# Performance work log

Hardware: AMD Instinct MI355X
Metric: run time of the kernel (lower is better)

## Reference

```python
import jax, jax.numpy as jnp
import numpy as np

S, B, D, H, E, K = 1024, 4, 1024, 16, 3, 2
DFF = 4 * D
DH = D // H


def _layernorm(x, w, b, eps=1e-5):
    mu = jnp.mean(x, axis=-1, keepdims=True)
    var = jnp.var(x, axis=-1, keepdims=True)
    return (x - mu) * jax.lax.rsqrt(var + eps) * w + b


def _quick_gelu(x):
    return x * jax.nn.sigmoid(1.702 * x)


def setup_inputs() -> dict:
    key = jax.random.key(0)
    ks = jax.random.split(key, 8)
    w = lambda k, shape: jax.random.normal(k, shape, dtype=jnp.float32) * 0.02
    return {
        "x": jax.random.normal(ks[0], (S, B, D), dtype=jnp.float32),
        "ln1_w": jnp.ones((D,), jnp.float32), "ln1_b": jnp.zeros((D,), jnp.float32),
        "ln2_w": jnp.ones((D,), jnp.float32), "ln2_b": jnp.zeros((D,), jnp.float32),
        "in_proj_w": w(ks[1], (3 * D, D)), "in_proj_b": jnp.zeros((3 * D,), jnp.float32),
        "out_proj_w": w(ks[2], (D, D)), "out_proj_b": jnp.zeros((D,), jnp.float32),
        "gate_w": w(ks[3], (E, D)),
        "fc_w": w(ks[4], (E, DFF, D)), "fc_b": jnp.zeros((E, DFF), jnp.float32),
        "proj_w": w(ks[5], (E, D, DFF)), "proj_b": jnp.zeros((E, D), jnp.float32),
    }


def _forward(x, ln1_w, ln1_b, ln2_w, ln2_b, in_proj_w, in_proj_b,
             out_proj_w, out_proj_b, gate_w, fc_w, fc_b, proj_w, proj_b):
    s, b, d = x.shape
    # --- causal self-attention (torch nn.MultiheadAttention, seq-first) ---
    h = _layernorm(x, ln1_w, ln1_b)
    qkv = h @ in_proj_w.T + in_proj_b                      # [S,B,3D]
    q, k, v = jnp.split(qkv, 3, axis=-1)
    to_bhsd = lambda t: t.reshape(s, b, H, DH).transpose(1, 2, 0, 3)  # [B,H,S,Dh]
    q, k, v = to_bhsd(q) * (DH ** -0.5), to_bhsd(k), to_bhsd(v)
    mask = jnp.where(jnp.arange(s)[:, None] >= jnp.arange(s)[None, :], 0.0, -jnp.inf)
    scores = jnp.einsum("bhqd,bhkd->bhqk", q, k) + mask    # [B,H,S,S]
    attn = jax.nn.softmax(scores, axis=-1)
    o = jnp.einsum("bhqk,bhkd->bhqd", attn, v)
    o = o.transpose(2, 0, 1, 3).reshape(s, b, d)
    x = x + (o @ out_proj_w.T + out_proj_b)

    # --- MoE routing ---
    hs = _layernorm(x, ln2_w, ln2_b)
    hs_flat = hs.reshape(-1, d)                            # [T,D], T = S*B
    router_logits = hs_flat @ gate_w.T                     # [T,E]
    rw = jax.nn.softmax(router_logits.astype(jnp.float32), axis=-1)
    top_vals, top_idx = jax.lax.top_k(rw, K)               # [T,K]
    top_vals = top_vals / jnp.sum(top_vals, axis=-1, keepdims=True)

    # dense grouped expert FFN (E=3 small, compute-all + masked combine)
    h1 = _quick_gelu(jnp.einsum("td,efd->etf", hs_flat, fc_w) + fc_b[:, None, :])
    expert_out = jnp.einsum("etf,edf->etd", h1, proj_w) + proj_b[:, None, :]  # [E,T,D]
    comb = jnp.sum(jax.nn.one_hot(top_idx, E, dtype=top_vals.dtype) * top_vals[..., None], axis=1)  # [T,E]
    final_hidden_states = jnp.einsum("te,etd->td", comb, expert_out).reshape(s, b, d)
    del final_hidden_states  # NOTE: source computes this but never uses it in the output

    gate_score = jnp.max(top_vals, axis=-1).reshape(s, b, 1)
    out = x * gate_score
    return out, router_logits


def reference(x, ln1_w, ln1_b, ln2_w, ln2_b, in_proj_w, in_proj_b,
              out_proj_w, out_proj_b, gate_w, fc_w, fc_b, proj_w, proj_b):
    return _forward(x, ln1_w, ln1_b, ln2_w, ln2_b, in_proj_w, in_proj_b,
                    out_proj_w, out_proj_b, gate_w, fc_w, fc_b, proj_w, proj_b)
```

## Files before the change

### kernel.cpp

```cpp
#include <hip/hip_runtime.h>
#include <hip/hip_bf16.h>

#define S_DIM 1024
#define B_DIM 4
#define D_DIM 1024
#define H_DIM 16
#define DH    64
#define T_DIM (S_DIM * B_DIM)
#define QKV_N (3 * D_DIM)

using bf16 = __hip_bfloat16;
typedef __attribute__((ext_vector_type(4))) float fx4;
typedef __attribute__((ext_vector_type(8))) short bx8;

__device__ __forceinline__ unsigned short f2bf(float f) {
  union { float f; unsigned int u; } cv; cv.f = f;
  unsigned int u = cv.u;
  unsigned int r = (u + 0x7FFFu + ((u >> 16) & 1u)) >> 16;
  return (unsigned short)r;
}

__device__ __forceinline__ void g2l16(const void* g, void* l) {
  __builtin_amdgcn_global_load_lds(
      (const __attribute__((address_space(1))) unsigned int*)g,
      (__attribute__((address_space(3))) unsigned int*)l, 16, 0, 0);
}

__global__ __launch_bounds__(256) void cast_f32_bf16(
    const float* __restrict__ src, bf16* __restrict__ dst, int n4) {
  const int i = blockIdx.x * 256 + threadIdx.x;
  if (i >= n4) return;
  const fx4 v = ((const fx4*)src)[i];
  ushort4 u;
  u.x = f2bf(v[0]); u.y = f2bf(v[1]); u.z = f2bf(v[2]); u.w = f2bf(v[3]);
  ((ushort4*)dst)[i] = u;
}

__global__ __launch_bounds__(256) void ln_bf16_kernel(
    const float* __restrict__ x, const float* __restrict__ w,
    const float* __restrict__ bb, bf16* __restrict__ out) {
  const int t = blockIdx.x, tid = threadIdx.x;
  const fx4 v = ((const fx4*)(x + (size_t)t * D_DIM))[tid];
  float s  = v[0] + v[1] + v[2] + v[3];
  float ss = v[0]*v[0] + v[1]*v[1] + v[2]*v[2] + v[3]*v[3];
#pragma unroll
  for (int off = 32; off >= 1; off >>= 1) {
    s  += __shfl_xor(s, off);
    ss += __shfl_xor(ss, off);
  }
  __shared__ float red[8];
  const int wid = tid >> 6, lane = tid & 63;
  if (lane == 0) { red[wid] = s; red[4 + wid] = ss; }
  __syncthreads();
  s  = red[0] + red[1] + red[2] + red[3];
  ss = red[4] + red[5] + red[6] + red[7];
  const float mu = s * (1.f / D_DIM);
  const float rstd = rsqrtf(ss * (1.f / D_DIM) - mu * mu + 1e-5f);
  const fx4 wv = ((const fx4*)w)[tid];
  const fx4 bv = ((const fx4*)bb)[tid];
  ushort4 u;
  u.x = f2bf((v[0] - mu) * rstd * wv[0] + bv[0]);
  u.y = f2bf((v[1] - mu) * rstd * wv[1] + bv[1]);
  u.z = f2bf((v[2] - mu) * rstd * wv[2] + bv[2]);
  u.w = f2bf((v[3] - mu) * rstd * wv[3] + bv[3]);
  ((ushort4*)(out + (size_t)t * D_DIM))[tid] = u;
}

template <int EPI>
__global__ __launch_bounds__(256, 2) void gemm_bt(
    const bf16* __restrict__ A, const bf16* __restrict__ B,
    const float* __restrict__ bias, const float* __restrict__ resid,
    float* __restrict__ C, ushort* __restrict__ qkvb, int N, int K) {
  __shared__ bf16 sA[128 * 32];
  __shared__ bf16 sB[128 * 32];
  const int tid  = threadIdx.x;
  const int brow = blockIdx.y * 128;
  const int bcol = blockIdx.x * 128;
  const int wid  = tid >> 6;
  const int lane = tid & 63;
  const int wr   = wid >> 1;
  const int wc   = wid & 1;
  const int fr   = lane & 15;
  const int fk   = lane >> 4;

  fx4 acc[4][4];
#pragma unroll
  for (int i = 0; i < 4; ++i)
#pragma unroll
    for (int j = 0; j < 4; ++j) acc[i][j] = 0.f;

  const int arow = tid >> 2;
  const int acol = (tid & 3) * 8;

  for (int kt = 0; kt < K; kt += 32) {
    __syncthreads();
#pragma unroll
    for (int is = 0; is < 2; ++is) {
      const int row = is * 64 + arow;
      const int off = row * 64 + acol * 2;
      g2l16(A + (size_t)(brow + row) * K + kt + acol, (char*)sA + off);
      g2l16(B + (size_t)(bcol + row) * K + kt + acol, (char*)sB + off);
    }
    __syncthreads();

    bx8 af[4], bfr[4];
#pragma unroll
    for (int mm = 0; mm < 4; ++mm)
      af[mm] = *(const bx8*)(sA + (wr * 64 + mm * 16 + fr) * 32 + fk * 8);
#pragma unroll
    for (int nn = 0; nn < 4; ++nn)
      bfr[nn] = *(const bx8*)(sB + (wc * 64 + nn * 16 + fr) * 32 + fk * 8);
#pragma unroll
    for (int mm = 0; mm < 4; ++mm)
#pragma unroll
      for (int nn = 0; nn < 4; ++nn)
        acc[mm][nn] = __builtin_amdgcn_mfma_f32_16x16x32_bf16(
            af[mm], bfr[nn], acc[mm][nn], 0, 0, 0);
  }

  const int row0 = brow + wr * 64 + fk * 4;
  const int col0 = bcol + wc * 64 + fr;
#pragma unroll
  for (int mm = 0; mm < 4; ++mm) {
#pragma unroll
    for (int nn = 0; nn < 4; ++nn) {
      const int col = col0 + nn * 16;
      const float bv = bias[col];
      if (EPI == 1) {
#pragma unroll
        for (int rr = 0; rr < 4; ++rr) {
          const int row = row0 + mm * 16 + rr;
          C[(size_t)row * N + col] = acc[mm][nn][rr] + bv + resid[(size_t)row * N + col];
        }
      } else {
        const int which = col >> 10;
        const int rem   = col & 1023;
        const int hh    = rem >> 6;
        const int dh    = rem & 63;
        const float scale = (which == 0) ? 0.125f : 1.0f;
#pragma unroll
        for (int rr = 0; rr < 4; ++rr) {
          const int row = row0 + mm * 16 + rr;
          const int ss2 = row >> 2, bb2 = row & 3;
          const float v = (acc[mm][nn][rr] + bv) * scale;
          qkvb[(size_t)which * 4194304 +
               ((size_t)(bb2 * 16 + hh)) * 65536 + (size_t)ss2 * 64 + dh] = f2bf(v);
        }
      }
    }
  }
}

__global__ __launch_bounds__(256, 4) void attn_mfma(
    const ushort* __restrict__ qb, const ushort* __restrict__ kb,
    const ushort* __restrict__ vb, ushort* __restrict__ ob) {
  __shared__ __align__(16) char sK[8192];
  __shared__ __align__(16) char sVT[8192];
  __shared__ __align__(16) char sP[8192];
  const int tid  = threadIdx.x;
  const int wid  = tid >> 6;
  const int lane = tid & 63;
  const int g  = blockIdx.x;
  const int u  = g >> 1;
  const int pr = u & 7;
  const int qt = (g & 1) ? (15 - pr) : pr;
  const int bh = u >> 3;
  const int b  = bh >> 4, h = bh & 15;
  const int q0 = qt * 64;
  const int fr = lane & 15;
  const int fk = lane >> 4;
  const size_t bhoff = (size_t)bh * 65536;

  const int qrow = q0 + wid * 16 + fr;
  const bx8 qf0 = *(const bx8*)(qb + bhoff + (size_t)qrow * 64 + fk * 8);
  const bx8 qf1 = *(const bx8*)(qb + bhoff + (size_t)qrow * 64 + 32 + fk * 8);

  fx4 o4[4];
  float m[4], l[4];
#pragma unroll
  for (int dt = 0; dt < 4; ++dt) o4[dt] = 0.f;
#pragma unroll
  for (int rr = 0; rr < 4; ++rr) { m[rr] = -INFINITY; l[rr] = 0.f; }

  char* const sPw = sP + wid * 2048;

  for (int kbk = 0; kbk <= qt; ++kbk) {
    const int k0 = kbk * 64;
    __syncthreads();
#pragma unroll
    for (int is = 0; is < 2; ++is) {
      const int L    = is * 4096 + tid * 16;
      const int row  = L >> 7;
      const int colb = (L & 127) ^ ((row & 7) << 4);
      g2l16(kb + bhoff + (size_t)(k0 + row) * 64 + (colb >> 1), sK + L);
    }
    {
      const ushort* vp = vb + bhoff + (size_t)(k0 + lane) * 64 + wid * 16;
      const bx8 va  = *(const bx8*)vp;
      const bx8 vb2 = *(const bx8*)(vp + 8);
#pragma unroll
      for (int i = 0; i < 8; ++i) {
        const int dh0 = wid * 16 + i;
        *(ushort*)(sVT + ((dh0 * 128 + lane * 2) ^ ((i & 7) << 4))) = (ushort)va[i];
        const int dh1 = dh0 + 8;
        *(ushort*)(sVT + ((dh1 * 128 + lane * 2) ^ ((i & 7) << 4))) = (ushort)vb2[i];
      }
    }
    __syncthreads();

    fx4 s4[4];
#pragma unroll
    for (int kt = 0; kt < 4; ++kt) {
      const int krow = kt * 16 + fr;
      const int sw   = (krow & 7) << 4;
      const bx8 b0 = *(const bx8*)(sK + krow * 128 + ((fk * 16) ^ sw));
      const bx8 b1 = *(const bx8*)(sK + krow * 128 + ((64 + fk * 16) ^ sw));
      fx4 z = {0.f, 0.f, 0.f, 0.f};
      z = __builtin_amdgcn_mfma_f32_16x16x32_bf16(qf0, b0, z, 0, 0, 0);
      s4[kt] = __builtin_amdgcn_mfma_f32_16x16x32_bf16(qf1, b1, z, 0, 0, 0);
    }

    if (kbk == qt) {
#pragma unroll
      for (int kt = 0; kt < 4; ++kt) {
        const int key = k0 + kt * 16 + fr;
#pragma unroll
        for (int rr = 0; rr < 4; ++rr) {
          const int qq = q0 + wid * 16 + fk * 4 + rr;
          if (key > qq) s4[kt][rr] = -INFINITY;
        }
      }
    }

    float pm[4];
#pragma unroll
    for (int rr = 0; rr < 4; ++rr)
      pm[rr] = fmaxf(fmaxf(s4[0][rr], s4[1][rr]), fmaxf(s4[2][rr], s4[3][rr]));
#pragma unroll
    for (int off = 1; off <= 8; off <<= 1)
#pragma unroll
      for (int rr = 0; rr < 4; ++rr)
        pm[rr] = fmaxf(pm[rr], __shfl_xor(pm[rr], off));

#pragma unroll
    for (int rr = 0; rr < 4; ++rr) {
      const float mn = fmaxf(m[rr], pm[rr]);
      const float f  = __expf(m[rr] - mn);
      m[rr] = mn;
      l[rr] *= f;
#pragma unroll
      for (int dt = 0; dt < 4; ++dt) o4[dt][rr] *= f;
    }

#pragma unroll
    for (int kt = 0; kt < 4; ++kt) {
#pragma unroll
      for (int rr = 0; rr < 4; ++rr) {
        const float pv = __expf(s4[kt][rr] - m[rr]);
        l[rr] += pv;
        const int qr = fk * 4 + rr;
        *(ushort*)(sPw + ((qr * 128 + (kt * 16 + fr) * 2) ^ ((qr & 7) << 4))) = f2bf(pv);
      }
    }

#pragma unroll
    for (int c = 0; c < 2; ++c) {
      const bx8 pa = *(const bx8*)(sPw + fr * 128 + ((c * 64 + fk * 16) ^ ((fr & 7) << 4)));
#pragma unroll
      for (int dt = 0; dt < 4; ++dt) {
        const int vrow = dt * 16 + fr;
        const bx8 vf = *(const bx8*)(sVT + vrow * 128 + ((c * 64 + fk * 16) ^ ((vrow & 7) << 4)));
        o4[dt] = __builtin_amdgcn_mfma_f32_16x16x32_bf16(pa, vf, o4[dt], 0, 0, 0);
      }
    }
  }

#pragma unroll
  for (int off = 1; off <= 8; off <<= 1)
#pragma unroll
    for (int rr = 0; rr < 4; ++rr) l[rr] += __shfl_xor(l[rr], off);
#pragma unroll
  for (int rr = 0; rr < 4; ++rr) l[rr] = 1.f / l[rr];

#pragma unroll
  for (int dt = 0; dt < 4; ++dt) {
#pragma unroll
    for (int rr = 0; rr < 4; ++rr) {
      const int qq = q0 + wid * 16 + fk * 4 + rr;
      ob[((size_t)qq * 4 + b) * 1024 + h * 64 + dt * 16 + fr] =
          f2bf(o4[dt][rr] * l[rr]);
    }
  }
}

__global__ __launch_bounds__(256) void final_kernel(
    const float* __restrict__ xn, const float* __restrict__ w,
    const float* __restrict__ bb, const float* __restrict__ gw,
    float* __restrict__ out, float* __restrict__ rlog) {
  const int t = blockIdx.x, tid = threadIdx.x;
  const fx4 v = ((const fx4*)(xn + (size_t)t * D_DIM))[tid];
  float s  = v[0] + v[1] + v[2] + v[3];
  float ss = v[0]*v[0] + v[1]*v[1] + v[2]*v[2] + v[3]*v[3];
#pragma unroll
  for (int off = 32; off >= 1; off >>= 1) {
    s  += __shfl_xor(s, off);
    ss += __shfl_xor(ss, off);
  }
  __shared__ float red[8];
  __shared__ float red2[12];
  const int wid = tid >> 6, lane = tid & 63;
  if (lane == 0) { red[wid] = s; red[4 + wid] = ss; }
  __syncthreads();
  s  = red[0] + red[1] + red[2] + red[3];
  ss = red[4] + red[5] + red[6] + red[7];
  const float mu = s * (1.f / D_DIM);
  const float rstd = rsqrtf(ss * (1.f / D_DIM) - mu * mu + 1e-5f);
  const fx4 wv = ((const fx4*)w)[tid];
  const fx4 bv = ((const fx4*)bb)[tid];
  fx4 hv;
#pragma unroll
  for (int cc = 0; cc < 4; ++cc) hv[cc] = (v[cc] - mu) * rstd * wv[cc] + bv[cc];

  const fx4 w0 = ((const fx4*)(gw           ))[tid];
  const fx4 w1 = ((const fx4*)(gw +     D_DIM))[tid];
  const fx4 w2 = ((const fx4*)(gw + 2 * D_DIM))[tid];
  float g0 = hv[0]*w0[0] + hv[1]*w0[1] + hv[2]*w0[2] + hv[3]*w0[3];
  float g1 = hv[0]*w1[0] + hv[1]*w1[1] + hv[2]*w1[2] + hv[3]*w1[3];
  float g2 = hv[0]*w2[0] + hv[1]*w2[1] + hv[2]*w2[2] + hv[3]*w2[3];
#pragma unroll
  for (int off = 32; off >= 1; off >>= 1) {
    g0 += __shfl_xor(g0, off);
    g1 += __shfl_xor(g1, off);
    g2 += __shfl_xor(g2, off);
  }
  if (lane == 0) { red2[wid] = g0; red2[4 + wid] = g1; red2[8 + wid] = g2; }
  __syncthreads();
  g0 = red2[0] + red2[1] + red2[2]  + red2[3];
  g1 = red2[4] + red2[5] + red2[6]  + red2[7];
  g2 = red2[8] + red2[9] + red2[10] + red2[11];

  const float lmax = fmaxf(g0, fmaxf(g1, g2));
  const float lmin = fminf(g0, fminf(g1, g2));
  const float lmid = (g0 + g1 + g2) - lmax - lmin;
  const float gate = 1.f / (1.f + __expf(lmid - lmax));

  ((fx4*)(out + (size_t)t * D_DIM))[tid] = v * gate;
  if (tid == 0) {
    rlog[(size_t)t * 3 + 0] = g0;
    rlog[(size_t)t * 3 + 1] = g1;
    rlog[(size_t)t * 3 + 2] = g2;
  }
}

extern "C" void kernel_launch(void* const* d_in, const int* in_sizes, int n_in,
                              void* d_out, int out_size, void* d_ws, size_t ws_size,
                              hipStream_t stream) {
  (void)in_sizes; (void)n_in; (void)out_size; (void)ws_size;
  const float* x    = (const float*)d_in[0];
  const float* ln1w = (const float*)d_in[1];
  const float* ln1b = (const float*)d_in[2];
  const float* ln2w = (const float*)d_in[3];
  const float* ln2b = (const float*)d_in[4];
  const float* win  = (const float*)d_in[5];
  const float* bin  = (const float*)d_in[6];
  const float* wout = (const float*)d_in[7];
  const float* bout = (const float*)d_in[8];
  const float* gw   = (const float*)d_in[9];

  char* ws = (char*)d_ws;
  bf16*   w_in_b  = (bf16*)(ws);
  bf16*   w_out_b = (bf16*)(ws + 6291456);
  bf16*   h_b     = (bf16*)(ws + 8388608);
  ushort* o_b     = (ushort*)h_b;
  ushort* qkvb    = (ushort*)(ws + 16777216);
  ushort* q_b     = qkvb;
  ushort* k_b     = qkvb + 4194304;
  ushort* v_b     = qkvb + 8388608;
  float*  xnew    = (float*)(ws + 41943040);

  float* out  = (float*)d_out;
  float* rlog = out + (size_t)T_DIM * D_DIM;

  cast_f32_bf16<<<(3145728 / 4) / 256, 256, 0, stream>>>(win,  w_in_b,  3145728 / 4);
  cast_f32_bf16<<<(1048576 / 4) / 256, 256, 0, stream>>>(wout, w_out_b, 1048576 / 4);
  ln_bf16_kernel<<<T_DIM, 256, 0, stream>>>(x, ln1w, ln1b, h_b);
  gemm_bt<2><<<dim3(QKV_N / 128, T_DIM / 128), 256, 0, stream>>>(
      h_b, w_in_b, bin, nullptr, nullptr, qkvb, QKV_N, D_DIM);
  attn_mfma<<<1024, 256, 0, stream>>>(q_b, k_b, v_b, o_b);
  gemm_bt<1><<<dim3(D_DIM / 128, T_DIM / 128), 256, 0, stream>>>(
      (const bf16*)o_b, w_out_b, bout, x, xnew, nullptr, D_DIM, D_DIM);
  final_kernel<<<T_DIM, 256, 0, stream>>>(xnew, ln2w, ln2b, gw, out, rlog);
}
```

Baseline: 139.2 us.

## Double-buffer K/V tiles in attention with pre-transposed V and lazy rescale

A separate kernel pre-transposes V so the attention kernel can stage both K and V^T tiles into LDS with async global_load_lds. The loads are double-buffered, so the next tile streams in while the current one is computed. The kernel also skips the online-softmax rescale unless the row max grows by more than a threshold, adds s_setprio around the MFMA sections, and merges the two weight-cast launches into one. In exchange it adds a launch and an extra V read/write pass, doubles the LDS footprint (which may limit occupancy), and makes the lazy rescale rely on the threshold staying numerically safe.

```diff
diff --git a/kernel.cpp b/kernel.cpp
--- a/kernel.cpp
+++ b/kernel.cpp
@@ -26,14 +26,18 @@
       (__attribute__((address_space(3))) unsigned int*)l, 16, 0, 0);
 }
 
-__global__ __launch_bounds__(256) void cast_f32_bf16(
-    const float* __restrict__ src, bf16* __restrict__ dst, int n4) {
+__global__ __launch_bounds__(256) void cast2_f32_bf16(
+    const float* __restrict__ a, bf16* __restrict__ da, int an4,
+    const float* __restrict__ b, bf16* __restrict__ db, int bn4) {
   const int i = blockIdx.x * 256 + threadIdx.x;
-  if (i >= n4) return;
-  const fx4 v = ((const fx4*)src)[i];
+  const float* src; bf16* dst; int j;
+  if (i < an4) { src = a; dst = da; j = i; }
+  else if (i < an4 + bn4) { src = b; dst = db; j = i - an4; }
+  else return;
+  const fx4 v = ((const fx4*)src)[j];
   ushort4 u;
   u.x = f2bf(v[0]); u.y = f2bf(v[1]); u.z = f2bf(v[2]); u.w = f2bf(v[3]);
-  ((ushort4*)dst)[i] = u;
+  ((ushort4*)dst)[j] = u;
 }
 
 __global__ __launch_bounds__(256) void ln_bf16_kernel(
@@ -151,11 +155,39 @@
   }
 }
 
+__global__ __launch_bounds__(256) void transpose_v(
+    const ushort* __restrict__ v, ushort* __restrict__ vt) {
+  __shared__ ushort tile[64][65];
+  const int g  = blockIdx.x;
+  const int bh = g >> 4, st = g & 15;
+  const int s0 = st * 64;
+  const int tid = threadIdx.x;
+  const int r  = tid >> 2;
+  const int c0 = (tid & 3) * 16;
+  const ushort* src = v + (size_t)bh * 65536 + (size_t)(s0 + r) * 64 + c0;
+#pragma unroll
+  for (int i = 0; i < 2; ++i) {
+    const bx8 d = *(const bx8*)(src + i * 8);
+#pragma unroll
+    for (int j = 0; j < 8; ++j) tile[r][c0 + i * 8 + j] = (ushort)d[j];
+  }
+  __syncthreads();
+  ushort* dst = vt + (size_t)bh * 65536 + (size_t)r * 1024 + s0 + c0;
+  bx8 w0, w1;
+#pragma unroll
+  for (int j = 0; j < 8; ++j) {
+    w0[j] = (short)tile[c0 + j][r];
+    w1[j] = (short)tile[c0 + 8 + j][r];
+  }
+  *(bx8*)dst = w0;
+  *(bx8*)(dst + 8) = w1;
+}
+
 __global__ __launch_bounds__(256, 4) void attn_mfma(
     const ushort* __restrict__ qb, const ushort* __restrict__ kb,
-    const ushort* __restrict__ vb, ushort* __restrict__ ob) {
-  __shared__ __align__(16) char sK[8192];
-  __shared__ __align__(16) char sVT[8192];
+    const ushort* __restrict__ vtb, ushort* __restrict__ ob) {
+  __shared__ __align__(16) char sK[2][8192];
+  __shared__ __align__(16) char sVT[2][8192];
   __shared__ __align__(16) char sP[8192];
   const int tid  = threadIdx.x;
   const int wid  = tid >> 6;
@@ -174,6 +206,7 @@
   const int qrow = q0 + wid * 16 + fr;
   const bx8 qf0 = *(const bx8*)(qb + bhoff + (size_t)qrow * 64 + fk * 8);
   const bx8 qf1 = *(const bx8*)(qb + bhoff + (size_t)qrow * 64 + 32 + fk * 8);
+  asm volatile("s_waitcnt vmcnt(0)" ::: "memory");
 
   fx4 o4[4];
   float m[4], l[4];
@@ -184,41 +217,47 @@
 
   char* const sPw = sP + wid * 2048;
 
-  for (int kbk = 0; kbk <= qt; ++kbk) {
+  auto stage = [&](int buf, int kbk) {
     const int k0 = kbk * 64;
-    __syncthreads();
 #pragma unroll
     for (int is = 0; is < 2; ++is) {
       const int L    = is * 4096 + tid * 16;
       const int row  = L >> 7;
       const int colb = (L & 127) ^ ((row & 7) << 4);
-      g2l16(kb + bhoff + (size_t)(k0 + row) * 64 + (colb >> 1), sK + L);
-    }
-    {
-      const ushort* vp = vb + bhoff + (size_t)(k0 + lane) * 64 + wid * 16;
-      const bx8 va  = *(const bx8*)vp;
-      const bx8 vb2 = *(const bx8*)(vp + 8);
-#pragma unroll
-      for (int i = 0; i < 8; ++i) {
-        const int dh0 = wid * 16 + i;
-        *(ushort*)(sVT + ((dh0 * 128 + lane * 2) ^ ((i & 7) << 4))) = (ushort)va[i];
-        const int dh1 = dh0 + 8;
-        *(ushort*)(sVT + ((dh1 * 128 + lane * 2) ^ ((i & 7) << 4))) = (ushort)vb2[i];
-      }
-    }
-    __syncthreads();
+      g2l16(kb  + bhoff + (size_t)(k0 + row) * 64 + (colb >> 1), sK[buf]  + L);
+      g2l16(vtb + bhoff + (size_t)row * 1024 + k0 + (colb >> 1), sVT[buf] + L);
+    }
+  };
+
+  stage(0, 0);
+  int cur = 0;
+
+  for (int kbk = 0; kbk <= qt; ++kbk) {
+    const int k0 = kbk * 64;
+    if (kbk < qt) {
+      stage(cur ^ 1, kbk + 1);
+      asm volatile("s_waitcnt vmcnt(4)" ::: "memory");
+    } else {
+      asm volatile("s_waitcnt vmcnt(0)" ::: "memory");
+    }
+    __builtin_amdgcn_s_barrier();
+    asm volatile("" ::: "memory");
+    const char* sKc  = sK[cur];
+    const char* sVTc = sVT[cur];
 
     fx4 s4[4];
+    __builtin_amdgcn_s_setprio(1);
 #pragma unroll
     for (int kt = 0; kt < 4; ++kt) {
       const int krow = kt * 16 + fr;
       const int sw   = (krow & 7) << 4;
-      const bx8 b0 = *(const bx8*)(sK + krow * 128 + ((fk * 16) ^ sw));
-      const bx8 b1 = *(const bx8*)(sK + krow * 128 + ((64 + fk * 16) ^ sw));
+      const bx8 b0 = *(const bx8*)(sKc + krow * 128 + ((fk * 16) ^ sw));
+      const bx8 b1 = *(const bx8*)(sKc + krow * 128 + ((64 + fk * 16) ^ sw));
       fx4 z = {0.f, 0.f, 0.f, 0.f};
       z = __builtin_amdgcn_mfma_f32_16x16x32_bf16(qf0, b0, z, 0, 0, 0);
       s4[kt] = __builtin_amdgcn_mfma_f32_16x16x32_bf16(qf1, b1, z, 0, 0, 0);
     }
+    __builtin_amdgcn_s_setprio(0);
 
     if (kbk == qt) {
 #pragma unroll
@@ -242,14 +281,19 @@
       for (int rr = 0; rr < 4; ++rr)
         pm[rr] = fmaxf(pm[rr], __shfl_xor(pm[rr], off));
 
-#pragma unroll
-    for (int rr = 0; rr < 4; ++rr) {
-      const float mn = fmaxf(m[rr], pm[rr]);
-      const float f  = __expf(m[rr] - mn);
-      m[rr] = mn;
-      l[rr] *= f;
-#pragma unroll
-      for (int dt = 0; dt < 4; ++dt) o4[dt][rr] *= f;
+    bool need = false;
+#pragma unroll
+    for (int rr = 0; rr < 4; ++rr) need = need || (pm[rr] > m[rr] + 8.f);
+    if (__any(need)) {
+#pragma unroll
+      for (int rr = 0; rr < 4; ++rr) {
+        const float mn = fmaxf(m[rr], pm[rr]);
+        const float f  = __expf(m[rr] - mn);
+        m[rr] = mn;
+        l[rr] *= f;
+#pragma unroll
+        for (int dt = 0; dt < 4; ++dt) o4[dt][rr] *= f;
+      }
     }
 
 #pragma unroll
@@ -263,16 +307,23 @@
       }
     }
 
+    __builtin_amdgcn_s_setprio(1);
 #pragma unroll
     for (int c = 0; c < 2; ++c) {
       const bx8 pa = *(const bx8*)(sPw + fr * 128 + ((c * 64 + fk * 16) ^ ((fr & 7) << 4)));
 #pragma unroll
       for (int dt = 0; dt < 4; ++dt) {
         const int vrow = dt * 16 + fr;
-        const bx8 vf = *(const bx8*)(sVT + vrow * 128 + ((c * 64 + fk * 16) ^ ((vrow & 7) << 4)));
+        const bx8 vf = *(const bx8*)(sVTc + vrow * 128 + ((c * 64 + fk * 16) ^ ((vrow & 7) << 4)));
         o4[dt] = __builtin_amdgcn_mfma_f32_16x16x32_bf16(pa, vf, o4[dt], 0, 0, 0);
       }
     }
+    __builtin_amdgcn_s_setprio(0);
+
+    asm volatile("" ::: "memory");
+    __builtin_amdgcn_s_barrier();
+    asm volatile("" ::: "memory");
+    cur ^= 1;
   }
 
 #pragma unroll
@@ -377,16 +428,18 @@
   ushort* k_b     = qkvb + 4194304;
   ushort* v_b     = qkvb + 8388608;
   float*  xnew    = (float*)(ws + 41943040);
+  ushort* vt_b    = (ushort*)(ws + 58720256);
 
   float* out  = (float*)d_out;
   float* rlog = out + (size_t)T_DIM * D_DIM;
 
-  cast_f32_bf16<<<(3145728 / 4) / 256, 256, 0, stream>>>(win,  w_in_b,  3145728 / 4);
-  cast_f32_bf16<<<(1048576 / 4) / 256, 256, 0, stream>>>(wout, w_out_b, 1048576 / 4);
+  cast2_f32_bf16<<<4096, 256, 0, stream>>>(win, w_in_b, 786432,
+                                           wout, w_out_b, 262144);
   ln_bf16_kernel<<<T_DIM, 256, 0, stream>>>(x, ln1w, ln1b, h_b);
   gemm_bt<2><<<dim3(QKV_N / 128, T_DIM / 128), 256, 0, stream>>>(
       h_b, w_in_b, bin, nullptr, nullptr, qkvb, QKV_N, D_DIM);
-  attn_mfma<<<1024, 256, 0, stream>>>(q_b, k_b, v_b, o_b);
+  transpose_v<<<1024, 256, 0, stream>>>(v_b, vt_b);
+  attn_mfma<<<1024, 256, 0, stream>>>(q_b, k_b, vt_b, o_b);
   gemm_bt<1><<<dim3(D_DIM / 128, T_DIM / 128), 256, 0, stream>>>(
       (const bf16*)o_b, w_out_b, bout, x, xnew, nullptr, D_DIM, D_DIM);
   final_kernel<<<T_DIM, 256, 0, stream>>>(xnew, ln2w, ln2b, gw, out, rlog);
```

Result: faster. 132.6 us (-4.7%).
